# Kernel tuning notes

Measured on AMD Instinct MI355X. Metric: run time of the kernel, lower is better.

The kernel has to match this reference:

```python
import jax, jax.numpy as jnp
import numpy as np

B, T, U = 4, 256, 64
D_ENC = D_PRED = 512
JOINT = 1024
VOCAB = 1024


def setup_inputs() -> dict:
    key = jax.random.key(0)
    ks = jax.random.split(key, 8)
    s = lambda d: 1.0 / np.sqrt(d)
    return {
        "enc": jax.random.normal(ks[0], (B, T, D_ENC), jnp.float32),
        "pred": jax.random.normal(ks[1], (B, U, D_PRED), jnp.float32),
        "W_enc": jax.random.normal(ks[2], (D_ENC, JOINT), jnp.float32) * s(D_ENC),
        "b_enc": jnp.zeros((JOINT,), jnp.float32),
        "W_pred": jax.random.normal(ks[3], (D_PRED, JOINT), jnp.float32) * s(D_PRED),
        "b_pred": jnp.zeros((JOINT,), jnp.float32),
        "W_out": jax.random.normal(ks[4], (JOINT, VOCAB), jnp.float32) * s(JOINT),
        "b_out": jnp.zeros((VOCAB,), jnp.float32),
    }


def reference(enc, pred, W_enc, b_enc, W_pred, b_pred, W_out, b_out):
    # Dense projections to joint_dim
    enc_out = jnp.einsum("btd,dj->btj", enc, W_enc) + b_enc      # [B,T,J]
    pred_out = jnp.einsum("bud,dj->buj", pred, W_pred) + b_pred  # [B,U,J]
    # Broadcast add over (T,U), tanh, then vocab projection
    joint = jnp.tanh(enc_out[:, :, None, :] + pred_out[:, None, :, :])  # [B,T,U,J]
    logits = jnp.einsum("btuj,jv->btuv", joint, W_out) + b_out           # [B,T,U,V]
    return logits
```

## Files before the change

### kernel.cpp

```cpp
#include <hip/hip_runtime.h>
#include <hip/hip_bf16.h>


typedef __bf16 bf16x8 __attribute__((ext_vector_type(8)));
typedef float f32x4 __attribute__((ext_vector_type(4)));
typedef unsigned int u32x4 __attribute__((ext_vector_type(4)));
using bf16_t = __hip_bfloat16;

#define B_ 4
#define T_ 256
#define U_ 64
#define DE 512
#define JD 1024
#define VV 1024

__device__ __forceinline__ void gl2lds16(const void* g, void* l) {
  __builtin_amdgcn_global_load_lds(
      (__attribute__((address_space(1))) void*)(g),
      (__attribute__((address_space(3))) void*)(l), 16, 0, 0);
}

__device__ __forceinline__ float fast_tanh(float x) {
  float xx = fminf(fmaxf(x, -30.f), 30.f);
  float e = __expf(2.f * xx);
  return 1.f - 2.f * __builtin_amdgcn_rcpf(e + 1.f);
}

__device__ __forceinline__ void transpose_body(const float* __restrict__ src,
                                               bf16_t* __restrict__ dst,
                                               int K, int N, int bx, int by, int tid,
                                               float (*tile)[33]) {
  const int nt = bx * 32, kt = by * 32;
  const int tx = tid & 31, ty = tid >> 5;
#pragma unroll
  for (int i = 0; i < 4; ++i)
    tile[ty + i * 8][tx] = src[(size_t)(kt + ty + i * 8) * N + nt + tx];
  __syncthreads();
#pragma unroll
  for (int i = 0; i < 4; ++i)
    dst[(size_t)(nt + ty + i * 8) * K + kt + tx] = __float2bfloat16(tile[tx][ty + i * 8]);
}

__global__ __launch_bounds__(256) void prep_k(
    const float* __restrict__ enc, const float* __restrict__ pred,
    bf16_t* __restrict__ encb, bf16_t* __restrict__ predb,
    const float* __restrict__ W_enc, bf16_t* __restrict__ WtE,
    const float* __restrict__ W_pred, bf16_t* __restrict__ WtP,
    const float* __restrict__ W_out, bf16_t* __restrict__ WtO) {
  __shared__ float tile[32][33];
  const int bid = blockIdx.x, tid = threadIdx.x;
  if (bid < 640) {
    size_t i = ((size_t)bid * 256 + tid) * 4;
    const float* src;
    bf16_t* dst;
    if (i < (size_t)B_ * T_ * DE) { src = enc; dst = encb; }
    else { i -= (size_t)B_ * T_ * DE; src = pred; dst = predb; }
    f32x4 v = *(const f32x4*)(src + i);
    bf16_t o[4];
#pragma unroll
    for (int z = 0; z < 4; ++z) o[z] = __float2bfloat16(v[z]);
    *(unsigned long long*)(dst + i) = *(unsigned long long*)o;
  } else if (bid < 1152) {
    const int lb = bid - 640;
    transpose_body(W_enc, WtE, DE, JD, lb & 31, lb >> 5, tid, tile);
  } else if (bid < 1664) {
    const int lb = bid - 1152;
    transpose_body(W_pred, WtP, DE, JD, lb & 31, lb >> 5, tid, tile);
  } else {
    const int lb = bid - 1664;
    transpose_body(W_out, WtO, JD, VV, lb & 31, lb >> 5, tid, tile);
  }
}

__device__ __forceinline__ void proj_body(const bf16_t* __restrict__ A,
                                          const bf16_t* __restrict__ Bt,
                                          const float* __restrict__ bias,
                                          float* __restrict__ C,
                                          int m0, int n0, int N, int K) {
  __shared__ bf16_t sA[128 * 32];
  __shared__ bf16_t sB[128 * 32];
  const int tid = threadIdx.x;
  const int wave = tid >> 6, lane = tid & 63;
  const int wm = wave >> 1, wn = wave & 1;

  f32x4 acc[4][4] = {};

  for (int k0 = 0; k0 < K; k0 += 32) {
    __syncthreads();
#pragma unroll
    for (int r = 0; r < 2; ++r) {
      const int base = (wave + 4 * r) * 1024;
      const int row  = (base >> 6) + (lane >> 2);
      const int kel  = (lane & 3) * 8;
      gl2lds16(A  + (size_t)(m0 + row) * K + k0 + kel, (char*)sA + base);
      gl2lds16(Bt + (size_t)(n0 + row) * K + k0 + kel, (char*)sB + base);
    }
    __syncthreads();
    bf16x8 af[4], bfr[4];
    const int kq = (lane >> 4) * 8;
#pragma unroll
    for (int i = 0; i < 4; ++i) {
      af[i]  = *(const bf16x8*)(const void*)(sA + (wm * 64 + i * 16 + (lane & 15)) * 32 + kq);
      bfr[i] = *(const bf16x8*)(const void*)(sB + (wn * 64 + i * 16 + (lane & 15)) * 32 + kq);
    }
#pragma unroll
    for (int i = 0; i < 4; ++i)
#pragma unroll
      for (int j = 0; j < 4; ++j)
        acc[i][j] = __builtin_amdgcn_mfma_f32_16x16x32_bf16(af[i], bfr[j], acc[i][j], 0, 0, 0);
  }

  float bv[4];
#pragma unroll
  for (int j = 0; j < 4; ++j) bv[j] = bias[n0 + wn * 64 + j * 16 + (lane & 15)];
#pragma unroll
  for (int i = 0; i < 4; ++i) {
    const int row = m0 + wm * 64 + i * 16 + ((lane >> 4) << 2);
#pragma unroll
    for (int j = 0; j < 4; ++j) {
      const int col = n0 + wn * 64 + j * 16 + (lane & 15);
#pragma unroll
      for (int rr = 0; rr < 4; ++rr)
        C[(size_t)(row + rr) * N + col] = acc[i][j][rr] + bv[j];
    }
  }
}

__global__ __launch_bounds__(256) void proj2_k(
    const bf16_t* __restrict__ encb, const bf16_t* __restrict__ predb,
    const bf16_t* __restrict__ WtE, const bf16_t* __restrict__ WtP,
    const float* __restrict__ b_enc, const float* __restrict__ b_pred,
    float* __restrict__ enc_o, float* __restrict__ pred_o) {
  int bid = blockIdx.x;
  if (bid < 64) {
    proj_body(encb, WtE, b_enc, enc_o, (bid >> 3) * 128, (bid & 7) * 128, JD, DE);
  } else {
    bid -= 64;
    proj_body(predb, WtP, b_pred, pred_o, (bid >> 3) * 128, (bid & 7) * 128, JD, DE);
  }
}

__global__ __launch_bounds__(256) void tanh_mat_k(
    const float* __restrict__ enc_o,
    const float* __restrict__ pred_o,
    bf16_t* __restrict__ joint) {
  size_t i = ((size_t)blockIdx.x * 256 + threadIdx.x) * 8;
  const int m = (int)(i >> 10);
  const int j = (int)(i & 1023);
  const int enc_row  = m >> 6;
  const int pred_row = ((m >> 14) << 6) | (m & 63);
  const f32x4* pe = (const f32x4*)(enc_o  + (size_t)enc_row  * JD + j);
  const f32x4* pp = (const f32x4*)(pred_o + (size_t)pred_row * JD + j);
  bf16_t vals[8];
#pragma unroll
  for (int q = 0; q < 2; ++q) {
    f32x4 e = pe[q], p = pp[q];
#pragma unroll
    for (int z = 0; z < 4; ++z)
      vals[q * 4 + z] = __float2bfloat16(fast_tanh(e[z] + p[z]));
  }
  *(u32x4*)(void*)(joint + i) = *(const u32x4*)(const void*)vals;
}


__global__ __launch_bounds__(512, 2) void vocab_gemm10_k(
    const bf16_t* __restrict__ A,
    const bf16_t* __restrict__ Bt,
    const float* __restrict__ bias,
    float* __restrict__ C) {
  __shared__ char smem[65536];
  const int tid  = threadIdx.x;
  const int wave = tid >> 6, lane = tid & 63;
  const int wm = wave >> 2, wn = wave & 3;

  const int cpx = gridDim.x >> 3;
  const int b   = blockIdx.x;
  const int lb  = (b & 7) * cpx + (b >> 3);
  const int n0  = (lb & 3) * 256;
  const int m0  = (lb >> 2) * 256;

  const int sr  = wave * 16 + (lane >> 2);
  const int scg = (lane & 3) ^ ((sr >> 1) & 3);
  const int ldst = wave * 1024 + lane * 16;
  const bf16_t* gA0 = A  + (size_t)(m0 + sr)       * JD + scg * 8;
  const bf16_t* gA1 = A  + (size_t)(m0 + 128 + sr) * JD + scg * 8;
  const bf16_t* gB0 = Bt + (size_t)(n0 + sr)       * JD + scg * 8;
  const bf16_t* gB1 = Bt + (size_t)(n0 + 128 + sr) * JD + scg * 8;

  const int sl = lane & 15, ql = lane >> 4;

  f32x4 acc[8][4] = {};
  bf16x8 af[4], bf[2];
  const int NT = JD / 32;

#define STAGE(D, H, S)                                                        \
  do {                                                                        \
    const bf16_t* g_ = ((H) == 0 ? gA0 : (H) == 1 ? gA1 : (H) == 2 ? gB0 : gB1) + (S) * 32; \
    gl2lds16(g_, smem + (D) * 32768 + (H) * 8192 + ldst);                     \
  } while (0)

#define LOAD_AF(D, QM)                                                        \
  do {                                                                        \
    _Pragma("unroll")                                                         \
    for (int i = 0; i < 4; ++i) {                                             \
      const int lr = (QM) * 64 + i * 16 + sl;                                 \
      af[i] = *(const bf16x8*)(const void*)(                                  \
          smem + (D) * 32768 + wm * 8192 + lr * 64 + ((ql ^ ((lr >> 1) & 3)) * 16)); \
    }                                                                         \
  } while (0)

#define LOAD_BF(D, QN)                                                        \
  do {                                                                        \
    _Pragma("unroll")                                                         \
    for (int jj = 0; jj < 2; ++jj) {                                          \
      const int lr = (wn & 1) * 64 + ((QN) * 2 + jj) * 16 + sl;               \
      bf[jj] = *(const bf16x8*)(const void*)(                                 \
          smem + (D) * 32768 + 16384 + (wn >> 1) * 8192 + lr * 64 +           \
          ((ql ^ ((lr >> 1) & 3)) * 16));                                     \
    }                                                                         \
  } while (0)

#define MFMA_Q(QM, QN)                                                        \
  do {                                                                        \
    __builtin_amdgcn_s_setprio(1);                                            \
    _Pragma("unroll")                                                         \
    for (int i = 0; i < 4; ++i)                                               \
      _Pragma("unroll")                                                       \
      for (int jj = 0; jj < 2; ++jj)                                          \
        acc[(QM) * 4 + i][(QN) * 2 + jj] = __builtin_amdgcn_mfma_f32_16x16x32_bf16( \
            af[i], bf[jj], acc[(QM) * 4 + i][(QN) * 2 + jj], 0, 0, 0);        \
    __builtin_amdgcn_s_setprio(0);                                            \
  } while (0)

#define BAR1()                                                                \
  do {                                                                        \
    __builtin_amdgcn_s_barrier();                                             \
    asm volatile("s_waitcnt lgkmcnt(0)" ::: "memory");                        \
    __builtin_amdgcn_sched_barrier(0);                                        \
  } while (0)

#define BAR2()                                                                \
  do {                                                                        \
    __builtin_amdgcn_s_barrier();                                             \
    __builtin_amdgcn_sched_barrier(0);                                        \
  } while (0)

#define STEP(D, S)                                                            \
  do {                                                                        \
    const int s_ = (S);                                                       \
                                                              \
    LOAD_AF(D, 0); LOAD_BF(D, 0);                                             \
    if (s_ + 1 < NT) STAGE((D) ^ 1, 2, s_ + 1);                               \
    BAR1(); MFMA_Q(0, 0); BAR2();                                             \
                                                              \
    LOAD_BF(D, 1);                                                            \
    if (s_ + 1 < NT) STAGE((D) ^ 1, 3, s_ + 1);                               \
    BAR1(); MFMA_Q(0, 1); BAR2();                                             \
                                                              \
    LOAD_AF(D, 1);                                                            \
    BAR1(); MFMA_Q(1, 1); BAR2();                                             \
                                                              \
    LOAD_BF(D, 0);                                                            \
    if (s_ + 2 < NT) { STAGE(D, 0, s_ + 2); STAGE(D, 1, s_ + 2); }            \
    BAR1(); MFMA_Q(1, 0);                                                     \
    if (s_ + 1 < NT) {                                                        \
      if (s_ + 2 < NT) asm volatile("s_waitcnt vmcnt(2)" ::: "memory");       \
      else             asm volatile("s_waitcnt vmcnt(0)" ::: "memory");       \
      BAR2();                                                                 \
    }                                                                         \
  } while (0)

  STAGE(0, 0, 0); STAGE(0, 1, 0); STAGE(0, 2, 0); STAGE(0, 3, 0);
  STAGE(1, 0, 1); STAGE(1, 1, 1);
  asm volatile("s_waitcnt vmcnt(2)" ::: "memory");
  __builtin_amdgcn_s_barrier();
  __builtin_amdgcn_sched_barrier(0);

  for (int it = 0; it < NT / 2; ++it) {
    STEP(0, 2 * it);
    STEP(1, 2 * it + 1);
  }

#undef STAGE
#undef LOAD_AF
#undef LOAD_BF
#undef MFMA_Q
#undef BAR1
#undef BAR2
#undef STEP

  float bv[4];
#pragma unroll
  for (int j = 0; j < 4; ++j) bv[j] = bias[n0 + wn * 64 + j * 16 + (lane & 15)];
#pragma unroll
  for (int i = 0; i < 8; ++i) {
    const int row = m0 + wm * 128 + i * 16 + ((lane >> 4) << 2);
#pragma unroll
    for (int j = 0; j < 4; ++j) {
      const int col = n0 + wn * 64 + j * 16 + (lane & 15);
#pragma unroll
      for (int rr = 0; rr < 4; ++rr)
        C[(size_t)(row + rr) * VV + col] = acc[i][j][rr] + bv[j];
    }
  }
}

extern "C" void kernel_launch(void* const* d_in, const int* in_sizes, int n_in,
                              void* d_out, int out_size, void* d_ws, size_t ws_size,
                              hipStream_t stream) {
  const float* enc    = (const float*)d_in[0];
  const float* pred   = (const float*)d_in[1];
  const float* W_enc  = (const float*)d_in[2];
  const float* b_enc  = (const float*)d_in[3];
  const float* W_pred = (const float*)d_in[4];
  const float* b_pred = (const float*)d_in[5];
  const float* W_out  = (const float*)d_in[6];
  const float* b_out  = (const float*)d_in[7];
  float* out = (float*)d_out;

  char* ws = (char*)d_ws;
  bf16_t* encb   = (bf16_t*)(ws + 0x000000);
  bf16_t* predb  = (bf16_t*)(ws + 0x100000);
  bf16_t* WtE    = (bf16_t*)(ws + 0x140000);
  bf16_t* WtP    = (bf16_t*)(ws + 0x240000);
  bf16_t* WtO    = (bf16_t*)(ws + 0x340000);
  float*  enc_o  = (float*) (ws + 0x540000);
  float*  pred_o = (float*) (ws + 0x940000);
  bf16_t* joint  = (bf16_t*)(ws + 0xA40000);

  prep_k<<<2688, 256, 0, stream>>>(enc, pred, encb, predb, W_enc, WtE, W_pred, WtP, W_out, WtO);
  proj2_k<<<80, 256, 0, stream>>>(encb, predb, WtE, WtP, b_enc, b_pred, enc_o, pred_o);
  tanh_mat_k<<<(B_*T_*U_) * JD / (8 * 256), 256, 0, stream>>>(enc_o, pred_o, joint);
  vocab_gemm10_k<<<dim3(((B_*T_*U_) / 256) * (VV / 256)), 512, 0, stream>>>(
      joint, WtO, b_out, out);
}
```

Measured before the change: 435.9 us.

## Add vocab GEMM variant with 64-wide K tiles using 128KB dynamic LDS

```diff
diff --git a/kernel.cpp b/kernel.cpp
--- a/kernel.cpp
+++ b/kernel.cpp
@@ -162,12 +162,9 @@
   *(u32x4*)(void*)(joint + i) = *(const u32x4*)(const void*)vals;
 }
 
-
 __global__ __launch_bounds__(512, 2) void vocab_gemm10_k(
-    const bf16_t* __restrict__ A,
-    const bf16_t* __restrict__ Bt,
-    const float* __restrict__ bias,
-    float* __restrict__ C) {
+    const bf16_t* __restrict__ A, const bf16_t* __restrict__ Bt,
+    const float* __restrict__ bias, float* __restrict__ C) {
   __shared__ char smem[65536];
   const int tid  = threadIdx.x;
   const int wave = tid >> 6, lane = tid & 63;
@@ -248,18 +245,14 @@
 #define STEP(D, S)                                                            \
   do {                                                                        \
     const int s_ = (S);                                                       \
-                                                              \
     LOAD_AF(D, 0); LOAD_BF(D, 0);                                             \
     if (s_ + 1 < NT) STAGE((D) ^ 1, 2, s_ + 1);                               \
     BAR1(); MFMA_Q(0, 0); BAR2();                                             \
-                                                              \
     LOAD_BF(D, 1);                                                            \
     if (s_ + 1 < NT) STAGE((D) ^ 1, 3, s_ + 1);                               \
     BAR1(); MFMA_Q(0, 1); BAR2();                                             \
-                                                              \
     LOAD_AF(D, 1);                                                            \
     BAR1(); MFMA_Q(1, 1); BAR2();                                             \
-                                                              \
     LOAD_BF(D, 0);                                                            \
     if (s_ + 2 < NT) { STAGE(D, 0, s_ + 2); STAGE(D, 1, s_ + 2); }            \
     BAR1(); MFMA_Q(1, 0);                                                     \
@@ -288,6 +281,164 @@
 #undef BAR1
 #undef BAR2
 #undef STEP
+
+  float bv[4];
+#pragma unroll
+  for (int j = 0; j < 4; ++j) bv[j] = bias[n0 + wn * 64 + j * 16 + (lane & 15)];
+#pragma unroll
+  for (int i = 0; i < 8; ++i) {
+    const int row = m0 + wm * 128 + i * 16 + ((lane >> 4) << 2);
+#pragma unroll
+    for (int j = 0; j < 4; ++j) {
+      const int col = n0 + wn * 64 + j * 16 + (lane & 15);
+#pragma unroll
+      for (int rr = 0; rr < 4; ++rr)
+        C[(size_t)(row + rr) * VV + col] = acc[i][j][rr] + bv[j];
+    }
+  }
+}
+
+
+__global__ __launch_bounds__(512, 2) void vocab_gemm11_k(
+    const bf16_t* __restrict__ A,
+    const bf16_t* __restrict__ Bt,
+    const float* __restrict__ bias,
+    float* __restrict__ C) {
+  extern __shared__ char smem[];
+  const int tid  = threadIdx.x;
+  const int wave = tid >> 6, lane = tid & 63;
+  const int wm = wave >> 2, wn = wave & 3;
+
+  const int cpx = gridDim.x >> 3;
+  const int b   = blockIdx.x;
+  const int lb  = (b & 7) * cpx + (b >> 3);
+  const int n0  = (lb & 3) * 256;
+  const int m0  = (lb >> 2) * 256;
+
+  const int r0  = tid >> 3;
+  const int cg  = (tid & 7) ^ (r0 & 7);
+  const int stid = tid * 16;
+  const bf16_t* gA0a = A  + (size_t)(m0 + r0)        * JD + cg * 8;
+  const bf16_t* gA0b = A  + (size_t)(m0 + 64 + r0)   * JD + cg * 8;
+  const bf16_t* gA1a = A  + (size_t)(m0 + 128 + r0)  * JD + cg * 8;
+  const bf16_t* gA1b = A  + (size_t)(m0 + 192 + r0)  * JD + cg * 8;
+  const bf16_t* gB0a = Bt + (size_t)(n0 + r0)        * JD + cg * 8;
+  const bf16_t* gB0b = Bt + (size_t)(n0 + 64 + r0)   * JD + cg * 8;
+  const bf16_t* gB1a = Bt + (size_t)(n0 + 128 + r0)  * JD + cg * 8;
+  const bf16_t* gB1b = Bt + (size_t)(n0 + 192 + r0)  * JD + cg * 8;
+
+  const int sl = lane & 15, ql = lane >> 4;
+
+  f32x4 acc[8][4] = {};
+  bf16x8 af[2][4], bf[2][2];
+  const int NT = JD / 64;
+
+#define STAGE(H, S)                                                           \
+  do {                                                                        \
+    char* lb_ = smem + ((S) & 1) * 65536 + (H) * 16384 + stid;                \
+    const bf16_t* ga_ = ((H) == 0 ? gA0a : (H) == 1 ? gA1a : (H) == 2 ? gB0a : gB1a) + (S) * 64; \
+    const bf16_t* gb_ = ((H) == 0 ? gA0b : (H) == 1 ? gA1b : (H) == 2 ? gB0b : gB1b) + (S) * 64; \
+    gl2lds16(ga_, lb_);                                                       \
+    gl2lds16(gb_, lb_ + 8192);                                                \
+  } while (0)
+
+#define LOAD_AF(D, QM)                                                        \
+  do {                                                                        \
+    _Pragma("unroll")                                                         \
+    for (int ks = 0; ks < 2; ++ks)                                            \
+      _Pragma("unroll")                                                       \
+      for (int i = 0; i < 4; ++i) {                                           \
+        const int lr = (QM) * 64 + i * 16 + sl;                               \
+        const int ck = (ks * 4 + ql) ^ (lr & 7);                              \
+        af[ks][i] = *(const bf16x8*)(const void*)(                            \
+            smem + (D) * 65536 + wm * 16384 + lr * 128 + ck * 16);            \
+      }                                                                       \
+  } while (0)
+
+#define LOAD_BF(D, QN)                                                        \
+  do {                                                                        \
+    _Pragma("unroll")                                                         \
+    for (int ks = 0; ks < 2; ++ks)                                            \
+      _Pragma("unroll")                                                       \
+      for (int jj = 0; jj < 2; ++jj) {                                        \
+        const int lr = (wn & 1) * 64 + ((QN) * 2 + jj) * 16 + sl;             \
+        const int ck = (ks * 4 + ql) ^ (lr & 7);                              \
+        bf[ks][jj] = *(const bf16x8*)(const void*)(                           \
+            smem + (D) * 65536 + 32768 + (wn >> 1) * 16384 + lr * 128 + ck * 16); \
+      }                                                                       \
+  } while (0)
+
+#define MFMA_Q(QM, QN)                                                        \
+  do {                                                                        \
+    __builtin_amdgcn_s_setprio(1);                                            \
+    _Pragma("unroll")                                                         \
+    for (int ks = 0; ks < 2; ++ks)                                            \
+      _Pragma("unroll")                                                       \
+      for (int i = 0; i < 4; ++i)                                             \
+        _Pragma("unroll")                                                     \
+        for (int jj = 0; jj < 2; ++jj)                                        \
+          acc[(QM) * 4 + i][(QN) * 2 + jj] = __builtin_amdgcn_mfma_f32_16x16x32_bf16( \
+              af[ks][i], bf[ks][jj], acc[(QM) * 4 + i][(QN) * 2 + jj], 0, 0, 0); \
+    __builtin_amdgcn_s_setprio(0);                                            \
+  } while (0)
+
+#define BARW()                                                                \
+  do {                                                                        \
+    __builtin_amdgcn_s_barrier();                                             \
+    asm volatile("s_waitcnt lgkmcnt(0)" ::: "memory");                        \
+    __builtin_amdgcn_sched_barrier(0);                                        \
+  } while (0)
+
+#define BARC()                                                                \
+  do {                                                                        \
+    __builtin_amdgcn_s_barrier();                                             \
+    __builtin_amdgcn_sched_barrier(0);                                        \
+  } while (0)
+
+#define TILE(D, S)                                                            \
+  do {                                                                        \
+    const int t_ = (S);                                                       \
+                                               \
+    LOAD_AF(D, 0); LOAD_BF(D, 0);                                             \
+    if (t_ + 1 < NT) STAGE(1, t_ + 1);                                        \
+    BARW(); MFMA_Q(0, 0); BARC();                                             \
+                                               \
+    LOAD_BF(D, 1);                                                            \
+    if (t_ + 1 < NT) STAGE(2, t_ + 1);                                        \
+    BARW(); MFMA_Q(0, 1); BARC();                                             \
+                                               \
+    LOAD_AF(D, 1);                                                            \
+    if (t_ + 1 < NT) STAGE(3, t_ + 1);                                        \
+    BARW(); MFMA_Q(1, 1); BARC();                                             \
+                       \
+    LOAD_BF(D, 0);                                                            \
+    if (t_ + 2 < NT) STAGE(0, t_ + 2);                                        \
+    BARW(); MFMA_Q(1, 0);                                                     \
+    if (t_ + 1 < NT) {                                                        \
+      if (t_ + 2 < NT) asm volatile("s_waitcnt vmcnt(2)" ::: "memory");       \
+      else             asm volatile("s_waitcnt vmcnt(0)" ::: "memory");       \
+      BARC();                                                                 \
+    }                                                                         \
+  } while (0)
+
+  STAGE(0, 0); STAGE(1, 0); STAGE(2, 0); STAGE(3, 0);
+  STAGE(0, 1);
+  asm volatile("s_waitcnt vmcnt(2)" ::: "memory");
+  __builtin_amdgcn_s_barrier();
+  __builtin_amdgcn_sched_barrier(0);
+
+  for (int it = 0; it < NT / 2; ++it) {
+    TILE(0, 2 * it);
+    TILE(1, 2 * it + 1);
+  }
+
+#undef STAGE
+#undef LOAD_AF
+#undef LOAD_BF
+#undef MFMA_Q
+#undef BARW
+#undef BARC
+#undef TILE
 
   float bv[4];
 #pragma unroll
@@ -331,6 +482,17 @@
   prep_k<<<2688, 256, 0, stream>>>(enc, pred, encb, predb, W_enc, WtE, W_pred, WtP, W_out, WtO);
   proj2_k<<<80, 256, 0, stream>>>(encb, predb, WtE, WtP, b_enc, b_pred, enc_o, pred_o);
   tanh_mat_k<<<(B_*T_*U_) * JD / (8 * 256), 256, 0, stream>>>(enc_o, pred_o, joint);
-  vocab_gemm10_k<<<dim3(((B_*T_*U_) / 256) * (VV / 256)), 512, 0, stream>>>(
-      joint, WtO, b_out, out);
-}
+  static int big_lds = -1;
+  if (big_lds < 0) {
+    big_lds = (hipFuncSetAttribute(reinterpret_cast<const void*>(vocab_gemm11_k),
+                                   hipFuncAttributeMaxDynamicSharedMemorySize,
+                                   131072) == hipSuccess) ? 1 : 0;
+  }
+  if (big_lds == 1) {
+    vocab_gemm11_k<<<dim3(((B_*T_*U_) / 256) * (VV / 256)), 512, 131072, stream>>>(
+        joint, WtO, b_out, out);
+  } else {
+    vocab_gemm10_k<<<dim3(((B_*T_*U_) / 256) * (VV / 256)), 512, 0, stream>>>(
+        joint, WtO, b_out, out);
+  }
+}
```

Result: faster. 427.1 us (-2.0%).

## Cut per-quarter barriers in vocab GEMM with double-buffered register fragments

Applied to the files above, without the earlier changes.

```diff
diff --git a/kernel.cpp b/kernel.cpp
--- a/kernel.cpp
+++ b/kernel.cpp
@@ -163,7 +163,7 @@
 }
 
 
-__global__ __launch_bounds__(512, 2) void vocab_gemm10_k(
+__global__ __launch_bounds__(512, 2) void vocab_gemm12_k(
     const bf16_t* __restrict__ A,
     const bf16_t* __restrict__ Bt,
     const float* __restrict__ bias,
@@ -190,8 +190,10 @@
   const int sl = lane & 15, ql = lane >> 4;
 
   f32x4 acc[8][4] = {};
-  bf16x8 af[4], bf[2];
+  bf16x8 af0v[4], af1v[4], bf0v[2], bf1v[2];
   const int NT = JD / 32;
+
+#define SB() __builtin_amdgcn_sched_barrier(0)
 
 #define STAGE(D, H, S)                                                        \
   do {                                                                        \
@@ -199,74 +201,67 @@
     gl2lds16(g_, smem + (D) * 32768 + (H) * 8192 + ldst);                     \
   } while (0)
 
-#define LOAD_AF(D, QM)                                                        \
+#define ISSUE_AF(D, QM, DST)                                                  \
   do {                                                                        \
     _Pragma("unroll")                                                         \
     for (int i = 0; i < 4; ++i) {                                             \
       const int lr = (QM) * 64 + i * 16 + sl;                                 \
-      af[i] = *(const bf16x8*)(const void*)(                                  \
+      (DST)[i] = *(const bf16x8*)(const void*)(                               \
           smem + (D) * 32768 + wm * 8192 + lr * 64 + ((ql ^ ((lr >> 1) & 3)) * 16)); \
     }                                                                         \
   } while (0)
 
-#define LOAD_BF(D, QN)                                                        \
+#define ISSUE_BF(D, QN, DST)                                                  \
   do {                                                                        \
     _Pragma("unroll")                                                         \
     for (int jj = 0; jj < 2; ++jj) {                                          \
       const int lr = (wn & 1) * 64 + ((QN) * 2 + jj) * 16 + sl;               \
-      bf[jj] = *(const bf16x8*)(const void*)(                                 \
+      (DST)[jj] = *(const bf16x8*)(const void*)(                              \
           smem + (D) * 32768 + 16384 + (wn >> 1) * 8192 + lr * 64 +           \
           ((ql ^ ((lr >> 1) & 3)) * 16));                                     \
     }                                                                         \
   } while (0)
 
-#define MFMA_Q(QM, QN)                                                        \
-  do {                                                                        \
-    __builtin_amdgcn_s_setprio(1);                                            \
+#define MFMA8(AF, BF, QM, QN)                                                 \
+  do {                                                                        \
     _Pragma("unroll")                                                         \
     for (int i = 0; i < 4; ++i)                                               \
       _Pragma("unroll")                                                       \
       for (int jj = 0; jj < 2; ++jj)                                          \
         acc[(QM) * 4 + i][(QN) * 2 + jj] = __builtin_amdgcn_mfma_f32_16x16x32_bf16( \
-            af[i], bf[jj], acc[(QM) * 4 + i][(QN) * 2 + jj], 0, 0, 0);        \
-    __builtin_amdgcn_s_setprio(0);                                            \
-  } while (0)
-
-#define BAR1()                                                                \
-  do {                                                                        \
-    __builtin_amdgcn_s_barrier();                                             \
-    asm volatile("s_waitcnt lgkmcnt(0)" ::: "memory");                        \
-    __builtin_amdgcn_sched_barrier(0);                                        \
-  } while (0)
-
-#define BAR2()                                                                \
-  do {                                                                        \
-    __builtin_amdgcn_s_barrier();                                             \
-    __builtin_amdgcn_sched_barrier(0);                                        \
+            (AF)[i], (BF)[jj], acc[(QM) * 4 + i][(QN) * 2 + jj], 0, 0, 0);    \
   } while (0)
 
 #define STEP(D, S)                                                            \
   do {                                                                        \
     const int s_ = (S);                                                       \
                                                               \
-    LOAD_AF(D, 0); LOAD_BF(D, 0);                                             \
     if (s_ + 1 < NT) STAGE((D) ^ 1, 2, s_ + 1);                               \
-    BAR1(); MFMA_Q(0, 0); BAR2();                                             \
+    ISSUE_AF(D, 0, af0v); ISSUE_BF(D, 0, bf0v); SB();                         \
+    ISSUE_BF(D, 1, bf1v); SB();                                               \
+    asm volatile("s_waitcnt lgkmcnt(2)" ::: "memory"); SB();                  \
+    __builtin_amdgcn_s_setprio(1); MFMA8(af0v, bf0v, 0, 0);                   \
+    __builtin_amdgcn_s_setprio(0); SB();                                      \
                                                               \
-    LOAD_BF(D, 1);                                                            \
     if (s_ + 1 < NT) STAGE((D) ^ 1, 3, s_ + 1);                               \
-    BAR1(); MFMA_Q(0, 1); BAR2();                                             \
-                                                              \
-    LOAD_AF(D, 1);                                                            \
-    BAR1(); MFMA_Q(1, 1); BAR2();                                             \
-                                                              \
-    LOAD_BF(D, 0);                                                            \
-    if (s_ + 2 < NT) { STAGE(D, 0, s_ + 2); STAGE(D, 1, s_ + 2); }            \
-    BAR1(); MFMA_Q(1, 0);                                                     \
+    ISSUE_AF(D, 1, af1v); SB();                                               \
+    asm volatile("s_waitcnt lgkmcnt(4)" ::: "memory"); SB();                  \
+    __builtin_amdgcn_s_setprio(1); MFMA8(af0v, bf1v, 0, 1);                   \
+    __builtin_amdgcn_s_setprio(0); SB();                                      \
+                            \
+    asm volatile("s_waitcnt lgkmcnt(0)" ::: "memory"); SB();                  \
+    __builtin_amdgcn_s_setprio(1); MFMA8(af1v, bf1v, 1, 1);                   \
+    MFMA8(af1v, bf0v, 1, 0); __builtin_amdgcn_s_setprio(0); SB();             \
+                                                                \
     if (s_ + 1 < NT) {                                                        \
-      if (s_ + 2 < NT) asm volatile("s_waitcnt vmcnt(2)" ::: "memory");       \
-      else             asm volatile("s_waitcnt vmcnt(0)" ::: "memory");       \
-      BAR2();                                                                 \
+      __builtin_amdgcn_s_barrier(); SB();                                     \
+      if (s_ + 2 < NT) {                                                      \
+        STAGE(D, 0, s_ + 2); STAGE(D, 1, s_ + 2);                             \
+        asm volatile("s_waitcnt vmcnt(2)" ::: "memory");                      \
+      } else {                                                                \
+        asm volatile("s_waitcnt vmcnt(0)" ::: "memory");                      \
+      }                                                                       \
+      __builtin_amdgcn_s_barrier(); SB();                                     \
     }                                                                         \
   } while (0)
 
@@ -274,20 +269,19 @@
   STAGE(1, 0, 1); STAGE(1, 1, 1);
   asm volatile("s_waitcnt vmcnt(2)" ::: "memory");
   __builtin_amdgcn_s_barrier();
-  __builtin_amdgcn_sched_barrier(0);
+  SB();
 
   for (int it = 0; it < NT / 2; ++it) {
     STEP(0, 2 * it);
     STEP(1, 2 * it + 1);
   }
 
+#undef STEP
+#undef MFMA8
+#undef ISSUE_BF
+#undef ISSUE_AF
 #undef STAGE
-#undef LOAD_AF
-#undef LOAD_BF
-#undef MFMA_Q
-#undef BAR1
-#undef BAR2
-#undef STEP
+#undef SB
 
   float bv[4];
 #pragma unroll
@@ -331,6 +325,6 @@
   prep_k<<<2688, 256, 0, stream>>>(enc, pred, encb, predb, W_enc, WtE, W_pred, WtP, W_out, WtO);
   proj2_k<<<80, 256, 0, stream>>>(encb, predb, WtE, WtP, b_enc, b_pred, enc_o, pred_o);
   tanh_mat_k<<<(B_*T_*U_) * JD / (8 * 256), 256, 0, stream>>>(enc_o, pred_o, joint);
-  vocab_gemm10_k<<<dim3(((B_*T_*U_) / 256) * (VV / 256)), 512, 0, stream>>>(
+  vocab_gemm12_k<<<dim3(((B_*T_*U_) / 256) * (VV / 256)), 512, 0, stream>>>(
       joint, WtO, b_out, out);
 }
```

Result: no change. 438.5 us (+0.6%).
